# Performance work log

Hardware: AMD Instinct MI355X
Metric: run time of the kernel (lower is better)

## Reference

```python
import jax, jax.numpy as jnp
import numpy as np

N = 8192
IN_F = 128
OUT_F = 64
ALPHA = 0.2  # LeakyReLU negative slope
EDGE_P = 0.02  # adjacency density
NEG_INF = -1e12


def setup_inputs() -> dict:
    key = jax.random.key(0)
    k1, k2, k3, k4 = jax.random.split(key, 4)
    input_h = jax.random.normal(k1, (N, IN_F), dtype=jnp.float32)
    # sparse-ish 0/1 adjacency mask, with self-loops so every softmax row is valid
    adj = (jax.random.uniform(k2, (N, N)) < EDGE_P).astype(jnp.float32)
    adj = adj + jnp.eye(N, dtype=jnp.float32)
    # xavier_uniform with gain 1.414 as in the torch init
    def xavier(k, shape, gain=1.414):
        fan_in, fan_out = shape[0], shape[1]
        bound = gain * np.sqrt(6.0 / (fan_in + fan_out))
        return jax.random.uniform(k, shape, jnp.float32, -bound, bound)
    W = xavier(k3, (IN_F, OUT_F))
    a = xavier(k4, (2 * OUT_F, 1))
    return {"input_h": input_h, "adj": adj, "W": W, "a": a}


def reference(input_h, adj, W, a):
    # Wh: [N, F]
    Wh = input_h @ W
    # e[i, j] = leakyrelu(a1 . Wh_i + a2 . Wh_j)  (decomposed, no N*N*2F concat)
    a1 = a[:OUT_F, 0]   # [F]
    a2 = a[OUT_F:, 0]   # [F]
    s_src = Wh @ a1     # [N]
    s_dst = Wh @ a2     # [N]
    e = jax.nn.leaky_relu(s_src[:, None] + s_dst[None, :], negative_slope=ALPHA)  # [N, N]
    att = jnp.where(adj > 0, e, NEG_INF)
    att = jax.nn.softmax(att, axis=1)
    # dropout is identity in eval mode (training=False)
    out_h = att @ Wh    # [N, F]
    return out_h
```

## Files before the change

### kernel.cpp

```cpp
#include <hip/hip_runtime.h>
#include <hip/hip_bf16.h>

#define N 8192
#define IN_F 128
#define OUT_F 64
#define ALPHA 0.2f
#define LOG2E 1.442695040888963f

typedef __attribute__((ext_vector_type(8))) short short8;
typedef __attribute__((ext_vector_type(4))) float f32x4;

__device__ __forceinline__ float cvt(float x) { return x; }
__device__ __forceinline__ float cvt(__hip_bfloat16 x) { return __bfloat162float(x); }

__device__ __forceinline__ bool probe_fp32(const void* adj) {
    unsigned int u = *(const unsigned int*)adj;
    return (u == 0x3F800000u) || (u == 0x40000000u);
}

__device__ __forceinline__ short f2bf(float x) {
    union { __hip_bfloat16 b; short s; } u;
    u.b = __float2bfloat16(x);
    return u.s;
}
__device__ __forceinline__ float bfbits2f(short s) {
    union { unsigned int u; float f; } v;
    v.u = ((unsigned int)(unsigned short)s) << 16;
    return v.f;
}

template <typename T>
__device__ __forceinline__ void k1_body(
    const T* __restrict__ h, const T* __restrict__ W, const T* __restrict__ a,
    unsigned short* __restrict__ WhF, float* __restrict__ s_src, float* __restrict__ s_dst,
    float (*hrow)[IN_F])
{
    const int tid  = threadIdx.x;
    const int w    = tid >> 6;
    const int lane = tid & 63;
    const int R0   = blockIdx.x * 16;

    float Wcol[IN_F];
    #pragma unroll
    for (int t = 0; t < IN_F; ++t)
        Wcol[t] = cvt(W[t * OUT_F + lane]);

    for (int idx = tid; idx < 16 * IN_F; idx += 256) {
        int r = idx >> 7, c = idx & 127;
        hrow[r][c] = cvt(h[(size_t)(R0 + r) * IN_F + c]);
    }
    __syncthreads();

    const float a1 = cvt(a[lane]);
    const float a2 = cvt(a[OUT_F + lane]);
    const int nt = lane >> 4, l15 = lane & 15;

    for (int rr = 0; rr < 4; ++rr) {
        const int rloc = w * 4 + rr;
        const int j    = R0 + rloc;
        float acc = 0.f;
        #pragma unroll
        for (int b = 0; b < 32; ++b) {
            const float4 hv = *(const float4*)&hrow[rloc][b * 4];
            acc = fmaf(hv.x, Wcol[b * 4 + 0], acc);
            acc = fmaf(hv.y, Wcol[b * 4 + 1], acc);
            acc = fmaf(hv.z, Wcol[b * 4 + 2], acc);
            acc = fmaf(hv.w, Wcol[b * 4 + 3], acc);
        }
        WhF[((size_t)(j >> 5) * 4 + nt) * 512 + ((j >> 3) & 3) * 128 + l15 * 8 + (j & 7)]
            = (unsigned short)f2bf(acc);

        float s1 = acc * a1, s2 = acc * a2;
        #pragma unroll
        for (int off = 32; off; off >>= 1) {
            s1 += __shfl_xor(s1, off, 64);
            s2 += __shfl_xor(s2, off, 64);
        }
        if (lane == 0) { s_src[j] = s1; s_dst[j] = s2; }
    }
}

__global__ __launch_bounds__(256) void gat_k1(
    const void* h, const void* W, const void* a, const void* adj,
    unsigned short* WhF, float* s_src, float* s_dst)
{
    __shared__ float hrow[16][IN_F];
    if (probe_fp32(adj))
        k1_body<float>((const float*)h, (const float*)W, (const float*)a,
                       WhF, s_src, s_dst, hrow);
    else
        k1_body<__hip_bfloat16>((const __hip_bfloat16*)h, (const __hip_bfloat16*)W,
                                (const __hip_bfloat16*)a, WhF, s_src, s_dst, hrow);
}

#define K2_WAVES 8
template <typename TADJ, bool OUT_F32>
__device__ __forceinline__ void k2_body(
    const TADJ* __restrict__ adj,
    const unsigned short* __restrict__ WhF,
    const float* __restrict__ s_src,
    const float* __restrict__ s_dst,
    void* __restrict__ outv,
    float (*Cpart)[16][65], float (*Lpart)[16])
{
    const int tid  = threadIdx.x;
    const int wave = tid >> 6;
    const int lane = tid & 63;
    const int quad = lane >> 4;
    const int l15  = lane & 15;
    const int R0   = blockIdx.x * 16;

    const int   row = R0 + l15;
    const float si  = s_src[row];
    const TADJ* __restrict__ arow = adj + (size_t)row * N;

    f32x4 acc[4];
    #pragma unroll
    for (int nt = 0; nt < 4; ++nt) acc[nt] = (f32x4)0.f;
    float ls = 0.f;

    const int jw = wave * 1024;

    for (int kt = 0; kt < 32; ++kt) {
        const int jq = jw + kt * 32 + quad * 8;

        unsigned int bits[8];
        if constexpr (sizeof(TADJ) == 4) {
            const uint4 b0 = *(const uint4*)(arow + jq);
            const uint4 b1 = *(const uint4*)(arow + jq + 4);
            bits[0] = b0.x; bits[1] = b0.y; bits[2] = b0.z; bits[3] = b0.w;
            bits[4] = b1.x; bits[5] = b1.y; bits[6] = b1.z; bits[7] = b1.w;
        } else {
            const uint4 a8 = *(const uint4*)(arow + jq);
            bits[0] = a8.x & 0xffffu; bits[1] = a8.x >> 16;
            bits[2] = a8.y & 0xffffu; bits[3] = a8.y >> 16;
            bits[4] = a8.z & 0xffffu; bits[5] = a8.z >> 16;
            bits[6] = a8.w & 0xffffu; bits[7] = a8.w >> 16;
        }

        const float4 sd0 = *(const float4*)(s_dst + jq);
        const float4 sd1 = *(const float4*)(s_dst + jq + 4);

        const unsigned short* tb = WhF + (size_t)(wave * 32 + kt) * 2048;
        short8 bfr[4];
        #pragma unroll
        for (int nt = 0; nt < 4; ++nt)
            bfr[nt] = *(const short8*)(tb + nt * 512 + lane * 8);

        const float sdv[8] = {sd0.x, sd0.y, sd0.z, sd0.w, sd1.x, sd1.y, sd1.z, sd1.w};

        short8 A;
        #pragma unroll
        for (int t = 0; t < 8; ++t) {
            float e = si + sdv[t];
            e = fmaxf(e, ALPHA * e);
            float p = (bits[t] != 0u) ? __builtin_exp2f(e * LOG2E) : 0.f;
            A[t] = f2bf(p);
            ls += bfbits2f(A[t]);
        }

        #pragma unroll
        for (int nt = 0; nt < 4; ++nt)
            acc[nt] = __builtin_amdgcn_mfma_f32_16x16x32_bf16(A, bfr[nt], acc[nt], 0, 0, 0);
    }

    ls += __shfl_xor(ls, 16, 64);
    ls += __shfl_xor(ls, 32, 64);
    if (quad == 0) Lpart[wave][l15] = ls;

    #pragma unroll
    for (int nt = 0; nt < 4; ++nt)
        #pragma unroll
        for (int reg = 0; reg < 4; ++reg)
            Cpart[wave][quad * 4 + reg][nt * 16 + l15] = acc[nt][reg];

    __syncthreads();

    for (int idx = tid; idx < 16 * OUT_F; idx += 512) {
        const int i = idx >> 6, f = idx & 63;
        float s = 0.f, l = 0.f;
        #pragma unroll
        for (int w = 0; w < K2_WAVES; ++w) {
            s += Cpart[w][i][f];
            l += Lpart[w][i];
        }
        const float v = s / l;
        if constexpr (OUT_F32)
            ((float*)outv)[(size_t)(R0 + i) * OUT_F + f] = v;
        else
            ((__hip_bfloat16*)outv)[(size_t)(R0 + i) * OUT_F + f] = __float2bfloat16(v);
    }
}

__global__ __launch_bounds__(512) void gat_k2(
    const void* adj, const unsigned short* WhF,
    const float* s_src, const float* s_dst, void* out)
{
    __shared__ float Cpart[K2_WAVES][16][65];
    __shared__ float Lpart[K2_WAVES][16];
    if (probe_fp32(adj))
        k2_body<float, true>((const float*)adj, WhF, s_src, s_dst, out, Cpart, Lpart);
    else
        k2_body<unsigned short, false>((const unsigned short*)adj, WhF, s_src, s_dst,
                                       out, Cpart, Lpart);
}

extern "C" void kernel_launch(void* const* d_in, const int* in_sizes, int n_in,
                              void* d_out, int out_size, void* d_ws, size_t ws_size,
                              hipStream_t stream) {
    const void* h   = d_in[0];
    const void* adj = d_in[1];
    const void* W   = d_in[2];
    const void* a   = d_in[3];

    char* ws = (char*)d_ws;
    unsigned short* WhF = (unsigned short*)ws;
    float* s_src = (float*)(ws + (size_t)OUT_F * N * 2);
    float* s_dst = s_src + N;

    gat_k1<<<N / 16, 256, 0, stream>>>(h, W, a, adj, WhF, s_src, s_dst);
    gat_k2<<<N / 16, 512, 0, stream>>>(adj, WhF, s_src, s_dst, d_out);
}
```

Measured before the change: 416.2 us.

## Precompute adjacency bitmask in separate pass and stage it in LDS

Adds a streaming pre-kernel that compresses the dense adjacency matrix into a 1-bit-per-entry mask. The attention kernel then loads its 16 rows of mask into shared memory once, instead of issuing wide global loads of the full adjacency inside its inner loop. The intent is to take the bulky, latency-heavy adjacency traffic out of the exp/MFMA loop and read it in a simple bandwidth-friendly kernel. The cost is an extra launch and an extra small global write and read of the mask. The exp is now computed unconditionally and masked by select, and the inner loop is unrolled by two.

```diff
diff --git a/kernel.cpp b/kernel.cpp
--- a/kernel.cpp
+++ b/kernel.cpp
@@ -27,6 +27,37 @@
     union { unsigned int u; float f; } v;
     v.u = ((unsigned int)(unsigned short)s) << 16;
     return v.f;
+}
+
+__global__ __launch_bounds__(256) void gat_k0(const void* adjv, unsigned char* __restrict__ mask)
+{
+    const size_t t0     = (size_t)blockIdx.x * 256 + threadIdx.x;
+    const size_t nb     = (size_t)N * N / 8;
+    const size_t stride = (size_t)gridDim.x * 256;
+    if (probe_fp32(adjv)) {
+        const uint4* adj = (const uint4*)adjv;
+        for (size_t b = t0; b < nb; b += stride) {
+            const uint4 v0 = adj[b * 2];
+            const uint4 v1 = adj[b * 2 + 1];
+            unsigned int m = 0;
+            m |= (v0.x ? 1u : 0u);  m |= (v0.y ? 2u : 0u);
+            m |= (v0.z ? 4u : 0u);  m |= (v0.w ? 8u : 0u);
+            m |= (v1.x ? 16u : 0u); m |= (v1.y ? 32u : 0u);
+            m |= (v1.z ? 64u : 0u); m |= (v1.w ? 128u : 0u);
+            mask[b] = (unsigned char)m;
+        }
+    } else {
+        const uint4* adj = (const uint4*)adjv;
+        for (size_t b = t0; b < nb; b += stride) {
+            const uint4 v = adj[b];
+            unsigned int m = 0;
+            m |= ((v.x & 0xffffu) ? 1u : 0u);  m |= ((v.x >> 16) ? 2u : 0u);
+            m |= ((v.y & 0xffffu) ? 4u : 0u);  m |= ((v.y >> 16) ? 8u : 0u);
+            m |= ((v.z & 0xffffu) ? 16u : 0u); m |= ((v.z >> 16) ? 32u : 0u);
+            m |= ((v.w & 0xffffu) ? 64u : 0u); m |= ((v.w >> 16) ? 128u : 0u);
+            mask[b] = (unsigned char)m;
+        }
+    }
 }
 
 template <typename T>
@@ -94,13 +125,15 @@
 }
 
 #define K2_WAVES 8
-template <typename TADJ, bool OUT_F32>
+#define MROW 1040
+template <bool OUT_F32>
 __device__ __forceinline__ void k2_body(
-    const TADJ* __restrict__ adj,
+    const unsigned char* __restrict__ mask,
     const unsigned short* __restrict__ WhF,
     const float* __restrict__ s_src,
     const float* __restrict__ s_dst,
     void* __restrict__ outv,
+    unsigned char (*mlds)[MROW],
     float (*Cpart)[16][65], float (*Lpart)[16])
 {
     const int tid  = threadIdx.x;
@@ -110,9 +143,18 @@
     const int l15  = lane & 15;
     const int R0   = blockIdx.x * 16;
 
+    {
+        const int r = tid >> 5;
+        const int c = (tid & 31) * 32;
+        const uint4 m0 = *(const uint4*)(mask + (size_t)(R0 + r) * (N / 8) + c);
+        const uint4 m1 = *(const uint4*)(mask + (size_t)(R0 + r) * (N / 8) + c + 16);
+        *(uint4*)&mlds[r][c]      = m0;
+        *(uint4*)&mlds[r][c + 16] = m1;
+    }
+    __syncthreads();
+
     const int   row = R0 + l15;
     const float si  = s_src[row];
-    const TADJ* __restrict__ arow = adj + (size_t)row * N;
 
     f32x4 acc[4];
     #pragma unroll
@@ -121,22 +163,12 @@
 
     const int jw = wave * 1024;
 
+    #pragma unroll 2
     for (int kt = 0; kt < 32; ++kt) {
         const int jq = jw + kt * 32 + quad * 8;
 
-        unsigned int bits[8];
-        if constexpr (sizeof(TADJ) == 4) {
-            const uint4 b0 = *(const uint4*)(arow + jq);
-            const uint4 b1 = *(const uint4*)(arow + jq + 4);
-            bits[0] = b0.x; bits[1] = b0.y; bits[2] = b0.z; bits[3] = b0.w;
-            bits[4] = b1.x; bits[5] = b1.y; bits[6] = b1.z; bits[7] = b1.w;
-        } else {
-            const uint4 a8 = *(const uint4*)(arow + jq);
-            bits[0] = a8.x & 0xffffu; bits[1] = a8.x >> 16;
-            bits[2] = a8.y & 0xffffu; bits[3] = a8.y >> 16;
-            bits[4] = a8.z & 0xffffu; bits[5] = a8.z >> 16;
-            bits[6] = a8.w & 0xffffu; bits[7] = a8.w >> 16;
-        }
+        const unsigned int mword = *(const unsigned int*)&mlds[l15][wave * 128 + kt * 4];
+        const unsigned int mbyte = (mword >> (quad * 8)) & 0xffu;
 
         const float4 sd0 = *(const float4*)(s_dst + jq);
         const float4 sd1 = *(const float4*)(s_dst + jq + 4);
@@ -154,7 +186,8 @@
         for (int t = 0; t < 8; ++t) {
             float e = si + sdv[t];
             e = fmaxf(e, ALPHA * e);
-            float p = (bits[t] != 0u) ? __builtin_exp2f(e * LOG2E) : 0.f;
+            float p = __builtin_exp2f(e * LOG2E);
+            p = ((mbyte >> t) & 1u) ? p : 0.f;
             A[t] = f2bf(p);
             ls += bfbits2f(A[t]);
         }
@@ -193,16 +226,16 @@
 }
 
 __global__ __launch_bounds__(512) void gat_k2(
-    const void* adj, const unsigned short* WhF,
+    const void* adj, const unsigned char* mask, const unsigned short* WhF,
     const float* s_src, const float* s_dst, void* out)
 {
+    __shared__ __align__(16) unsigned char mlds[16][MROW];
     __shared__ float Cpart[K2_WAVES][16][65];
     __shared__ float Lpart[K2_WAVES][16];
     if (probe_fp32(adj))
-        k2_body<float, true>((const float*)adj, WhF, s_src, s_dst, out, Cpart, Lpart);
+        k2_body<true>(mask, WhF, s_src, s_dst, out, mlds, Cpart, Lpart);
     else
-        k2_body<unsigned short, false>((const unsigned short*)adj, WhF, s_src, s_dst,
-                                       out, Cpart, Lpart);
+        k2_body<false>(mask, WhF, s_src, s_dst, out, mlds, Cpart, Lpart);
 }
 
 extern "C" void kernel_launch(void* const* d_in, const int* in_sizes, int n_in,
@@ -214,10 +247,12 @@
     const void* a   = d_in[3];
 
     char* ws = (char*)d_ws;
-    unsigned short* WhF = (unsigned short*)ws;
-    float* s_src = (float*)(ws + (size_t)OUT_F * N * 2);
-    float* s_dst = s_src + N;
-
+    unsigned short* WhF  = (unsigned short*)ws;
+    float* s_src         = (float*)(ws + (1u << 20));
+    float* s_dst         = s_src + N;
+    unsigned char* mask  = (unsigned char*)(ws + (2u << 20));
+
+    gat_k0<<<2048, 256, 0, stream>>>(adj, mask);
     gat_k1<<<N / 16, 256, 0, stream>>>(h, W, a, adj, WhF, s_src, s_dst);
-    gat_k2<<<N / 16, 512, 0, stream>>>(adj, WhF, s_src, s_dst, d_out);
-}
+    gat_k2<<<N / 16, 512, 0, stream>>>(adj, mask, WhF, s_src, s_dst, d_out);
+}
```

After: 412.5 us. Within noise of the previous version (-0.9%).

## Stage adjacency as LDS bitmasks with register prefetch and coalesced row loads

Applied to the files above, without the earlier changes.

Each thread now loads 32 contiguous adjacency entries from one row with wide vector loads, packs them into a 32-bit mask, and stores it in a double-buffered LDS tile. The next chunk is prefetched into registers while the MFMA loop runs. The goal is coalesced, latency-hidden streaming of the 256MB adjacency matrix, which dominates runtime. In exchange it adds a __syncthreads per chunk, extra bit packing, and a larger register footprint for the prefetch buffer.

```diff
diff --git a/kernel.cpp b/kernel.cpp
--- a/kernel.cpp
+++ b/kernel.cpp
@@ -101,6 +101,7 @@
     const float* __restrict__ s_src,
     const float* __restrict__ s_dst,
     void* __restrict__ outv,
+    unsigned int (*mlds)[16][33],
     float (*Cpart)[16][65], float (*Lpart)[16])
 {
     const int tid  = threadIdx.x;
@@ -110,58 +111,93 @@
     const int l15  = lane & 15;
     const int R0   = blockIdx.x * 16;
 
-    const int   row = R0 + l15;
-    const float si  = s_src[row];
-    const TADJ* __restrict__ arow = adj + (size_t)row * N;
+    const int srow = tid >> 5;
+    const int sw   = tid & 31;
+
+    const float si = s_src[R0 + l15];
 
     f32x4 acc[4];
     #pragma unroll
     for (int nt = 0; nt < 4; ++nt) acc[nt] = (f32x4)0.f;
     float ls = 0.f;
 
-    const int jw = wave * 1024;
-
-    for (int kt = 0; kt < 32; ++kt) {
-        const int jq = jw + kt * 32 + quad * 8;
-
-        unsigned int bits[8];
+    constexpr int NPF = (sizeof(TADJ) == 4) ? 8 : 4;
+    uint4 pf[NPF];
+    const TADJ* __restrict__ abase = adj + (size_t)(R0 + srow) * N + sw * 32;
+
+    {
+        const uint4* p = (const uint4*)abase;
+        #pragma unroll
+        for (int k = 0; k < NPF; ++k) pf[k] = p[k];
+    }
+
+    for (int c = 0; c < 8; ++c) {
+        unsigned int word = 0;
         if constexpr (sizeof(TADJ) == 4) {
-            const uint4 b0 = *(const uint4*)(arow + jq);
-            const uint4 b1 = *(const uint4*)(arow + jq + 4);
-            bits[0] = b0.x; bits[1] = b0.y; bits[2] = b0.z; bits[3] = b0.w;
-            bits[4] = b1.x; bits[5] = b1.y; bits[6] = b1.z; bits[7] = b1.w;
+            #pragma unroll
+            for (int k = 0; k < 8; ++k) {
+                word |= (pf[k].x ? 1u : 0u) << (k * 4 + 0);
+                word |= (pf[k].y ? 1u : 0u) << (k * 4 + 1);
+                word |= (pf[k].z ? 1u : 0u) << (k * 4 + 2);
+                word |= (pf[k].w ? 1u : 0u) << (k * 4 + 3);
+            }
         } else {
-            const uint4 a8 = *(const uint4*)(arow + jq);
-            bits[0] = a8.x & 0xffffu; bits[1] = a8.x >> 16;
-            bits[2] = a8.y & 0xffffu; bits[3] = a8.y >> 16;
-            bits[4] = a8.z & 0xffffu; bits[5] = a8.z >> 16;
-            bits[6] = a8.w & 0xffffu; bits[7] = a8.w >> 16;
-        }
-
-        const float4 sd0 = *(const float4*)(s_dst + jq);
-        const float4 sd1 = *(const float4*)(s_dst + jq + 4);
-
-        const unsigned short* tb = WhF + (size_t)(wave * 32 + kt) * 2048;
-        short8 bfr[4];
-        #pragma unroll
-        for (int nt = 0; nt < 4; ++nt)
-            bfr[nt] = *(const short8*)(tb + nt * 512 + lane * 8);
-
-        const float sdv[8] = {sd0.x, sd0.y, sd0.z, sd0.w, sd1.x, sd1.y, sd1.z, sd1.w};
-
-        short8 A;
-        #pragma unroll
-        for (int t = 0; t < 8; ++t) {
-            float e = si + sdv[t];
-            e = fmaxf(e, ALPHA * e);
-            float p = (bits[t] != 0u) ? __builtin_exp2f(e * LOG2E) : 0.f;
-            A[t] = f2bf(p);
-            ls += bfbits2f(A[t]);
-        }
-
-        #pragma unroll
-        for (int nt = 0; nt < 4; ++nt)
-            acc[nt] = __builtin_amdgcn_mfma_f32_16x16x32_bf16(A, bfr[nt], acc[nt], 0, 0, 0);
+            #pragma unroll
+            for (int k = 0; k < 4; ++k) {
+                word |= ((pf[k].x & 0xffffu) ? 1u : 0u) << (k * 8 + 0);
+                word |= ((pf[k].x >> 16)     ? 1u : 0u) << (k * 8 + 1);
+                word |= ((pf[k].y & 0xffffu) ? 1u : 0u) << (k * 8 + 2);
+                word |= ((pf[k].y >> 16)     ? 1u : 0u) << (k * 8 + 3);
+                word |= ((pf[k].z & 0xffffu) ? 1u : 0u) << (k * 8 + 4);
+                word |= ((pf[k].z >> 16)     ? 1u : 0u) << (k * 8 + 5);
+                word |= ((pf[k].w & 0xffffu) ? 1u : 0u) << (k * 8 + 6);
+                word |= ((pf[k].w >> 16)     ? 1u : 0u) << (k * 8 + 7);
+            }
+        }
+        mlds[c & 1][srow][sw] = word;
+        __syncthreads();
+
+        if (c < 7) {
+            const uint4* p = (const uint4*)(abase + (c + 1) * 1024);
+            #pragma unroll
+            for (int k = 0; k < NPF; ++k) pf[k] = p[k];
+        }
+
+        #pragma unroll
+        for (int kt = 0; kt < 4; ++kt) {
+            const int w4kt = wave * 4 + kt;
+            const int jq   = c * 1024 + w4kt * 32 + quad * 8;
+
+            const unsigned int mword = mlds[c & 1][l15][w4kt];
+            const unsigned int mbyte = (mword >> (quad * 8)) & 0xffu;
+
+            const float4 sd0 = *(const float4*)(s_dst + jq);
+            const float4 sd1 = *(const float4*)(s_dst + jq + 4);
+
+            const unsigned short* tb = WhF + (size_t)(c * 32 + w4kt) * 2048;
+            short8 bfr[4];
+            #pragma unroll
+            for (int nt = 0; nt < 4; ++nt)
+                bfr[nt] = *(const short8*)(tb + nt * 512 + lane * 8);
+
+            const float sdv[8] = {sd0.x, sd0.y, sd0.z, sd0.w, sd1.x, sd1.y, sd1.z, sd1.w};
+
+            short8 A;
+            #pragma unroll
+            for (int t = 0; t < 8; ++t) {
+                float e = si + sdv[t];
+                e = fmaxf(e, ALPHA * e);
+                float p = __builtin_exp2f(e * LOG2E);
+                p = ((mbyte >> t) & 1u) ? p : 0.f;
+                A[t] = f2bf(p);
+                ls += bfbits2f(A[t]);
+            }
+
+            #pragma unroll
+            for (int nt = 0; nt < 4; ++nt)
+                acc[nt] = __builtin_amdgcn_mfma_f32_16x16x32_bf16(A, bfr[nt], acc[nt], 0, 0, 0);
+        }
+        __syncthreads();
     }
 
     ls += __shfl_xor(ls, 16, 64);
@@ -196,13 +232,15 @@
     const void* adj, const unsigned short* WhF,
     const float* s_src, const float* s_dst, void* out)
 {
+    __shared__ unsigned int mlds[2][16][33];
     __shared__ float Cpart[K2_WAVES][16][65];
     __shared__ float Lpart[K2_WAVES][16];
     if (probe_fp32(adj))
-        k2_body<float, true>((const float*)adj, WhF, s_src, s_dst, out, Cpart, Lpart);
+        k2_body<float, true>((const float*)adj, WhF, s_src, s_dst, out,
+                             mlds, Cpart, Lpart);
     else
         k2_body<unsigned short, false>((const unsigned short*)adj, WhF, s_src, s_dst,
-                                       out, Cpart, Lpart);
+                                       out, mlds, Cpart, Lpart);
 }
 
 extern "C" void kernel_launch(void* const* d_in, const int* in_sizes, int n_in,
@@ -215,8 +253,8 @@
 
     char* ws = (char*)d_ws;
     unsigned short* WhF = (unsigned short*)ws;
-    float* s_src = (float*)(ws + (size_t)OUT_F * N * 2);
-    float* s_dst = s_src + N;
+    float* s_src        = (float*)(ws + (1u << 20));
+    float* s_dst        = s_src + N;
 
     gat_k1<<<N / 16, 256, 0, stream>>>(h, W, a, adj, WhF, s_src, s_dst);
     gat_k2<<<N / 16, 512, 0, stream>>>(adj, WhF, s_src, s_dst, d_out);
```

New measurement: 432.0 us. 3.8% more time.

## Pre-pack adjacency rows into LDS bitmasks with coalesced loads and ballots

Applied to the files above, without the earlier changes.

Each block first streams its 16 adjacency rows with lane-contiguous coalesced loads and converts them via wave ballots into a 256-word bitmask per row in LDS. The main MFMA loop then reads one mask word per step instead of strided 32-byte per-lane global loads. LOG2E is folded into the stored source/destination scores so the loop skips a multiply, and the workspace offset for the score arrays is moved. Adds a prologue phase and a barrier before compute, which serialises adjacency streaming with the MFMA work instead of overlapping it.

```diff
diff --git a/kernel.cpp b/kernel.cpp
--- a/kernel.cpp
+++ b/kernel.cpp
@@ -76,7 +76,7 @@
             s1 += __shfl_xor(s1, off, 64);
             s2 += __shfl_xor(s2, off, 64);
         }
-        if (lane == 0) { s_src[j] = s1; s_dst[j] = s2; }
+        if (lane == 0) { s_src[j] = s1 * LOG2E; s_dst[j] = s2 * LOG2E; }
     }
 }
 
@@ -101,6 +101,7 @@
     const float* __restrict__ s_src,
     const float* __restrict__ s_dst,
     void* __restrict__ outv,
+    unsigned int (*mlds)[257],
     float (*Cpart)[16][65], float (*Lpart)[16])
 {
     const int tid  = threadIdx.x;
@@ -110,9 +111,44 @@
     const int l15  = lane & 15;
     const int R0   = blockIdx.x * 16;
 
-    const int   row = R0 + l15;
-    const float si  = s_src[row];
-    const TADJ* __restrict__ arow = adj + (size_t)row * N;
+    #pragma unroll
+    for (int rr = 0; rr < 2; ++rr) {
+        const int r = wave * 2 + rr;
+        if constexpr (sizeof(TADJ) == 4) {
+            const unsigned int* rowp = (const unsigned int*)adj + (size_t)(R0 + r) * N + lane;
+            for (int c0 = 0; c0 < 128; c0 += 8) {
+                unsigned int v[8];
+                #pragma unroll
+                for (int k = 0; k < 8; ++k) v[k] = rowp[(c0 + k) * 64];
+                #pragma unroll
+                for (int k = 0; k < 8; ++k) {
+                    unsigned long long b = __ballot(v[k] != 0u);
+                    if (lane == 0) {
+                        mlds[r][(c0 + k) * 2]     = (unsigned int)b;
+                        mlds[r][(c0 + k) * 2 + 1] = (unsigned int)(b >> 32);
+                    }
+                }
+            }
+        } else {
+            const unsigned short* rowp = (const unsigned short*)adj + (size_t)(R0 + r) * N + lane;
+            for (int c0 = 0; c0 < 128; c0 += 8) {
+                unsigned short v[8];
+                #pragma unroll
+                for (int k = 0; k < 8; ++k) v[k] = rowp[(c0 + k) * 64];
+                #pragma unroll
+                for (int k = 0; k < 8; ++k) {
+                    unsigned long long b = __ballot(v[k] != 0);
+                    if (lane == 0) {
+                        mlds[r][(c0 + k) * 2]     = (unsigned int)b;
+                        mlds[r][(c0 + k) * 2 + 1] = (unsigned int)(b >> 32);
+                    }
+                }
+            }
+        }
+    }
+    __syncthreads();
+
+    const float si = s_src[R0 + l15];
 
     f32x4 acc[4];
     #pragma unroll
@@ -121,22 +157,12 @@
 
     const int jw = wave * 1024;
 
+    #pragma unroll 2
     for (int kt = 0; kt < 32; ++kt) {
         const int jq = jw + kt * 32 + quad * 8;
 
-        unsigned int bits[8];
-        if constexpr (sizeof(TADJ) == 4) {
-            const uint4 b0 = *(const uint4*)(arow + jq);
-            const uint4 b1 = *(const uint4*)(arow + jq + 4);
-            bits[0] = b0.x; bits[1] = b0.y; bits[2] = b0.z; bits[3] = b0.w;
-            bits[4] = b1.x; bits[5] = b1.y; bits[6] = b1.z; bits[7] = b1.w;
-        } else {
-            const uint4 a8 = *(const uint4*)(arow + jq);
-            bits[0] = a8.x & 0xffffu; bits[1] = a8.x >> 16;
-            bits[2] = a8.y & 0xffffu; bits[3] = a8.y >> 16;
-            bits[4] = a8.z & 0xffffu; bits[5] = a8.z >> 16;
-            bits[6] = a8.w & 0xffffu; bits[7] = a8.w >> 16;
-        }
+        const unsigned int mword = mlds[l15][wave * 32 + kt];
+        const unsigned int mbyte = (mword >> (quad * 8)) & 0xffu;
 
         const float4 sd0 = *(const float4*)(s_dst + jq);
         const float4 sd1 = *(const float4*)(s_dst + jq + 4);
@@ -154,7 +180,8 @@
         for (int t = 0; t < 8; ++t) {
             float e = si + sdv[t];
             e = fmaxf(e, ALPHA * e);
-            float p = (bits[t] != 0u) ? __builtin_exp2f(e * LOG2E) : 0.f;
+            float p = __builtin_exp2f(e);
+            p = ((mbyte >> t) & 1u) ? p : 0.f;
             A[t] = f2bf(p);
             ls += bfbits2f(A[t]);
         }
@@ -196,13 +223,15 @@
     const void* adj, const unsigned short* WhF,
     const float* s_src, const float* s_dst, void* out)
 {
+    __shared__ unsigned int mlds[16][257];
     __shared__ float Cpart[K2_WAVES][16][65];
     __shared__ float Lpart[K2_WAVES][16];
     if (probe_fp32(adj))
-        k2_body<float, true>((const float*)adj, WhF, s_src, s_dst, out, Cpart, Lpart);
+        k2_body<float, true>((const float*)adj, WhF, s_src, s_dst, out,
+                             mlds, Cpart, Lpart);
     else
         k2_body<unsigned short, false>((const unsigned short*)adj, WhF, s_src, s_dst,
-                                       out, Cpart, Lpart);
+                                       out, mlds, Cpart, Lpart);
 }
 
 extern "C" void kernel_launch(void* const* d_in, const int* in_sizes, int n_in,
@@ -215,8 +244,8 @@
 
     char* ws = (char*)d_ws;
     unsigned short* WhF = (unsigned short*)ws;
-    float* s_src = (float*)(ws + (size_t)OUT_F * N * 2);
-    float* s_dst = s_src + N;
+    float* s_src        = (float*)(ws + (1u << 20));
+    float* s_dst        = s_src + N;
 
     gat_k1<<<N / 16, 256, 0, stream>>>(h, W, a, adj, WhF, s_src, s_dst);
     gat_k2<<<N / 16, 512, 0, stream>>>(adj, WhF, s_src, s_dst, d_out);
```

Result: faster. 406.6 us (-2.3%).
